# Kernel tuning notes

Hardware: AMD Instinct MI355X
Metric: run time of the kernel (lower is better)

## Reference

```python
import jax, jax.numpy as jnp
import numpy as np

# Mamba2 config (matches mamba_ssm.Mamba2 defaults used by the wrapper)
D_MODEL = 1024
D_STATE = 128
D_CONV = 4
EXPAND = 2
HEADDIM = 64
CHUNK = 256
D_INNER = EXPAND * D_MODEL            # 2048
NHEADS = D_INNER // HEADDIM           # 32
CONV_DIM = D_INNER + 2 * D_STATE      # 2304 (x, B, C share the causal conv)
D_IN_PROJ = 2 * D_INNER + 2 * D_STATE + NHEADS  # z, xBC, dt
EPS = 1e-5


def rmsnorm(x, w, eps=EPS):
    return x * jax.lax.rsqrt(jnp.mean(x * x, axis=-1, keepdims=True) + eps) * w


def setup_inputs() -> dict:
    key = jax.random.key(0)
    ks = jax.random.split(key, 8)
    B, L = 2, 2048
    def w(k, shape, sc=0.02):
        return jax.random.normal(k, shape, jnp.float32) * sc
    return {
        "x": jax.random.normal(ks[0], (B, L, D_MODEL), jnp.float32),
        "norm_w": jnp.ones((D_MODEL,), jnp.float32),
        "in_proj_w": w(ks[1], (D_IN_PROJ, D_MODEL)),
        "conv_w": w(ks[2], (CONV_DIM, 1, D_CONV), 0.2),   # depthwise kernel
        "conv_b": jnp.zeros((CONV_DIM,), jnp.float32),
        "dt_bias": w(ks[3], (NHEADS,), 1.0),
        "A_log": jnp.log(1.0 + 15.0 * jax.random.uniform(ks[4], (NHEADS,), jnp.float32)),
        "D": jnp.ones((NHEADS,), jnp.float32),
        "gnorm_w": jnp.ones((D_INNER,), jnp.float32),
        "out_proj_w": w(ks[5], (D_MODEL, D_INNER)),
    }


def _ssd(xd, a, Bm, Cm):
    """Chunked SSD scan (ssd_minimal_discrete).
    xd: (b,l,h,p) = x*dt ; a: (b,l,h) = dt*A ; Bm,Cm: (b,l,n) (ngroups=1)."""
    b, l, h, p = xd.shape
    n = Bm.shape[-1]
    nc = l // CHUNK
    xd = xd.reshape(b, nc, CHUNK, h, p)
    a = a.reshape(b, nc, CHUNK, h).transpose(0, 3, 1, 2)   # (b,h,nc,c)
    Bm = Bm.reshape(b, nc, CHUNK, n)
    Cm = Cm.reshape(b, nc, CHUNK, n)
    a_cs = jnp.cumsum(a, axis=-1)                           # (b,h,nc,c)
    # 1) intra-chunk: causal decay matrix L[t,s] = exp(sum_{s<i<=t} a_i)
    diff = a_cs[..., :, None] - a_cs[..., None, :]          # (b,h,nc,c,c)
    mask = jnp.tril(jnp.ones((CHUNK, CHUNK), bool))
    Lm = jnp.exp(jnp.where(mask, diff, 0.0)) * mask
    Y_diag = jnp.einsum("bcln,bcsn,bhcls,bcshp->bclhp", Cm, Bm, Lm, xd)
    # 2) per-chunk end states
    decay_states = jnp.exp(a_cs[..., -1:] - a_cs)           # (b,h,nc,c)
    states = jnp.einsum("bcln,bhcl,bclhp->bchpn", Bm, decay_states, xd)
    # 3) inter-chunk recurrence (vectorized segsum over the 8+1 chunk totals)
    tot = jnp.pad(a_cs[..., -1], ((0, 0), (0, 0), (1, 0)))  # (b,h,nc+1)
    tot_cs = jnp.cumsum(tot, axis=-1)
    dchunk = tot_cs[..., :, None] - tot_cs[..., None, :]    # (b,h,nc+1,nc+1)
    cmask = jnp.tril(jnp.ones((nc + 1, nc + 1), bool))
    dchunk = jnp.exp(jnp.where(cmask, dchunk, 0.0)) * cmask
    states = jnp.concatenate([jnp.zeros_like(states[:, :1]), states], axis=1)
    new_states = jnp.einsum("bhzc,bchpn->bzhpn", dchunk, states)
    init_states = new_states[:, :-1]                        # state entering each chunk
    # 4) state -> output contribution
    Y_off = jnp.einsum("bcln,bchpn,bhcl->bclhp", Cm, init_states, jnp.exp(a_cs))
    return (Y_diag + Y_off).reshape(b, l, h, p)


def reference(x, norm_w, in_proj_w, conv_w, conv_b, dt_bias, A_log, D, gnorm_w, out_proj_w):
    res = x
    u = rmsnorm(x, norm_w)
    zxbcdt = u @ in_proj_w.T                                # (b,l,d_in_proj)
    z, xBC, dt = jnp.split(zxbcdt, [D_INNER, D_INNER + CONV_DIM], axis=-1)
    # causal depthwise conv1d over (x,B,C), then SiLU
    xBC_t = jnp.pad(xBC.transpose(0, 2, 1), ((0, 0), (0, 0), (D_CONV - 1, 0)))
    conv = jax.lax.conv_general_dilated(
        xBC_t, conv_w, (1,), "VALID",
        dimension_numbers=("NCH", "OIH", "NCH"), feature_group_count=CONV_DIM)
    xBC = jax.nn.silu(conv.transpose(0, 2, 1) + conv_b)
    xs, Bm, Cm = jnp.split(xBC, [D_INNER, D_INNER + D_STATE], axis=-1)
    dt = jax.nn.softplus(dt + dt_bias)                      # (b,l,h)
    A = -jnp.exp(A_log)                                     # (h,)
    xh = xs.reshape(xs.shape[0], xs.shape[1], NHEADS, HEADDIM)
    y = _ssd(xh * dt[..., None], dt * A, Bm, Cm)
    y = y + D[None, None, :, None] * xh                     # skip term
    y = y.reshape(xs.shape)
    y = rmsnorm(y * jax.nn.silu(z), gnorm_w)                # gated RMSNorm
    return res + y @ out_proj_w.T
```

## Files before the change

kernel.cpp:

```cpp
#include <hip/hip_runtime.h>
#include <hip/hip_bf16.h>

typedef __hip_bfloat16 bf16_t;
typedef __attribute__((ext_vector_type(8))) short bfrag8;
typedef __attribute__((ext_vector_type(4))) float floatx4;

#define DM     1024
#define DI     2048
#define NHD    32
#define HD     64
#define DSTATE 128
#define CONVD  2304
#define NPROJ  4384
#define NPAD   4480
#define MR     4096
#define LL     2048
#define EPSF   1e-5f
#define PSTR   40
#define LOG2E  1.44269504088896f

__device__ __forceinline__ void gl_lds16(const void* g, void* l) {
  __builtin_amdgcn_global_load_lds((const __attribute__((address_space(1))) void*)g,
                                   (__attribute__((address_space(3))) void*)l, 16, 0, 0);
}
__device__ __forceinline__ unsigned pack_bf16_rn(float a, float b) {
  unsigned ua = (__float_as_uint(a) + 0x8000u) >> 16;
  unsigned ub = (__float_as_uint(b) + 0x8000u) >> 16;
  return ua | (ub << 16);
}
__device__ __forceinline__ unsigned short bf16u(float a) {
  return (unsigned short)((__float_as_uint(a) + 0x8000u) >> 16);
}
__device__ __forceinline__ float blo(unsigned u){ return __uint_as_float(u << 16); }
__device__ __forceinline__ float bhi(unsigned u){ return __uint_as_float(u & 0xffff0000u); }
__device__ __forceinline__ void unp8(uint4 u, float* v) {
  v[0]=blo(u.x); v[1]=bhi(u.x); v[2]=blo(u.y); v[3]=bhi(u.y);
  v[4]=blo(u.z); v[5]=bhi(u.z); v[6]=blo(u.w); v[7]=bhi(u.w);
}

__global__ void rms1_kernel(const float* __restrict__ x, const float* __restrict__ w,
                            bf16_t* __restrict__ ub) {
  int row = blockIdx.x, t = threadIdx.x;
  float4 v = ((const float4*)(x + (long)row * DM))[t];
  float ss = v.x*v.x + v.y*v.y + v.z*v.z + v.w*v.w;
#pragma unroll
  for (int off = 32; off > 0; off >>= 1) ss += __shfl_down(ss, off, 64);
  __shared__ float red[4];
  if ((t & 63) == 0) red[t >> 6] = ss;
  __syncthreads();
  float tot = red[0] + red[1] + red[2] + red[3];
  float rs = rsqrtf(tot * (1.f / DM) + EPSF);
  float4 wv = ((const float4*)w)[t];
  bf16_t* o = ub + (long)row * DM + t * 4;
  o[0] = __float2bfloat16(v.x * rs * wv.x);
  o[1] = __float2bfloat16(v.y * rs * wv.y);
  o[2] = __float2bfloat16(v.z * rs * wv.z);
  o[3] = __float2bfloat16(v.w * rs * wv.w);
}

#define W1CNT (NPAD * DM / 4)
#define W2CNT (DM * DI / 4)
__global__ void cvtw_kernel(const float* __restrict__ w1, const float* __restrict__ w2,
                            const float* __restrict__ gw,
                            bf16_t* __restrict__ o1, bf16_t* __restrict__ o2) {
  int i4 = blockIdx.x * 256 + threadIdx.x;
  if (i4 < W1CNT) {
    int idx = i4 * 4;
    int row = idx >> 10;
    float4 v = make_float4(0.f, 0.f, 0.f, 0.f);
    if (row < NPROJ) v = *(const float4*)(w1 + idx);
    bf16_t* d = o1 + idx;
    d[0] = __float2bfloat16(v.x); d[1] = __float2bfloat16(v.y);
    d[2] = __float2bfloat16(v.z); d[3] = __float2bfloat16(v.w);
  } else {
    int idx = (i4 - W1CNT) * 4;
    int k = idx & (DI - 1);
    float4 v = *(const float4*)(w2 + idx);
    float4 g = *(const float4*)(gw + k);
    bf16_t* d = o2 + idx;
    d[0] = __float2bfloat16(v.x * g.x); d[1] = __float2bfloat16(v.y * g.y);
    d[2] = __float2bfloat16(v.z * g.z); d[3] = __float2bfloat16(v.w * g.w);
  }
}

template<int TN, bool DO_RES, bool OUT_BF16>
__global__ __launch_bounds__(256) void gemm64_kernel(const bf16_t* __restrict__ A,
    const bf16_t* __restrict__ Bw, const float* __restrict__ resid,
    const float* __restrict__ rs_row, void* __restrict__ Cout, int N, int K) {
  __shared__ bf16_t As[128 * 64];
  __shared__ bf16_t Bs[TN * 64];
  const int tid = threadIdx.x;
  const int lane = tid & 63;
  const int wv = tid >> 6;
  const int l15 = lane & 15;
  const int l4 = lane >> 4;
  constexpr int MF = (TN == 128) ? 4 : 2;
  const int wm = (TN == 128) ? ((wv >> 1) << 6) : (wv << 5);
  const int wn = (TN == 128) ? ((wv & 1) << 6) : 0;
  const int tm = blockIdx.x << 7;
  const int tn = blockIdx.y * TN;

  floatx4 acc[MF][4];
#pragma unroll
  for (int i = 0; i < MF; i++)
#pragma unroll
    for (int j = 0; j < 4; j++) acc[i][j] = (floatx4){0.f, 0.f, 0.f, 0.f};

  const int r = tid >> 3;
  const int c8 = tid & 7;
  const int scol = ((c8 ^ (r & 7)) << 3);
  const bf16_t* Ag = A + (long)(tm + r) * K + scol;
  const bf16_t* Bg = Bw + (long)(tn + r) * K + scol;
  const int swz = l15 & 7;

  for (int k0 = 0; k0 < K; k0 += 64) {
#pragma unroll
    for (int q = 0; q < 4; q++)
      gl_lds16(Ag + (long)(q * 32) * K + k0, &As[q * 2048 + tid * 8]);
#pragma unroll
    for (int q = 0; q < TN / 32; q++)
      gl_lds16(Bg + (long)(q * 32) * K + k0, &Bs[q * 2048 + tid * 8]);
    __syncthreads();
#pragma unroll
    for (int kk = 0; kk < 2; kk++) {
      bfrag8 af[MF], bfr[4];
      const int ch = ((kk << 2) | l4) ^ swz;
#pragma unroll
      for (int j = 0; j < 4; j++)
        bfr[j] = *(const bfrag8*)&Bs[(wn + j * 16 + l15) * 64 + ch * 8];
#pragma unroll
      for (int i = 0; i < MF; i++)
        af[i] = *(const bfrag8*)&As[(wm + i * 16 + l15) * 64 + ch * 8];
#pragma unroll
      for (int i = 0; i < MF; i++)
#pragma unroll
        for (int j = 0; j < 4; j++)
          acc[i][j] = __builtin_amdgcn_mfma_f32_16x16x32_bf16(af[i], bfr[j], acc[i][j], 0, 0, 0);
    }
    __syncthreads();
  }
#pragma unroll
  for (int i = 0; i < MF; i++)
#pragma unroll
    for (int j = 0; j < 4; j++)
#pragma unroll
      for (int r2 = 0; r2 < 4; r2++) {
        int row = tm + wm + i * 16 + l4 * 4 + r2;
        int col = tn + wn + j * 16 + l15;
        float v = acc[i][j][r2];
        if (OUT_BF16) {
          ((bf16_t*)Cout)[(long)row * N + col] = __float2bfloat16(v);
        } else {
          if (DO_RES) v = v * rs_row[row] + resid[(long)row * N + col];
          ((float*)Cout)[(long)row * N + col] = v;
        }
      }
}

__global__ __launch_bounds__(256) void gemm_s_kernel(const bf16_t* __restrict__ Cmh,
                const bf16_t* __restrict__ Bmh, float* __restrict__ SL) {
  __shared__ bf16_t As[128 * 32];
  __shared__ bf16_t Bs[128 * 32];
  const int tid = threadIdx.x;
  const int lane = tid & 63;
  const int wv = tid >> 6;
  const int wm = (wv >> 1) << 6;
  const int wn = (wv & 1) << 6;
  const int bc = blockIdx.z;
  const int tm = blockIdx.x << 7;
  const int tn = blockIdx.y << 7;
  const int l15 = lane & 15;
  const int l4 = lane >> 4;
  floatx4 acc[4][4];
#pragma unroll
  for (int i = 0; i < 4; i++)
#pragma unroll
    for (int j = 0; j < 4; j++) acc[i][j] = (floatx4){0.f, 0.f, 0.f, 0.f};
  const int arow = tid >> 2;
  const int acol = (tid & 3) << 3;
  const bf16_t* Ag = Cmh + (long)bc * 256 * DSTATE + (long)(tm + arow) * DSTATE + acol;
  const bf16_t* Bg = Bmh + (long)bc * 256 * DSTATE + (long)(tn + arow) * DSTATE + acol;
  const long k64 = (long)64 * DSTATE;
  for (int k0 = 0; k0 < DSTATE; k0 += 32) {
    gl_lds16(Ag + k0, &As[tid * 8]);
    gl_lds16(Ag + k64 + k0, &As[2048 + tid * 8]);
    gl_lds16(Bg + k0, &Bs[tid * 8]);
    gl_lds16(Bg + k64 + k0, &Bs[2048 + tid * 8]);
    __syncthreads();
    bfrag8 af[4], bfr[4];
#pragma unroll
    for (int i = 0; i < 4; i++)
      af[i] = *(const bfrag8*)&As[(wm + i * 16 + l15) * 32 + l4 * 8];
#pragma unroll
    for (int j = 0; j < 4; j++)
      bfr[j] = *(const bfrag8*)&Bs[(wn + j * 16 + l15) * 32 + l4 * 8];
#pragma unroll
    for (int i = 0; i < 4; i++)
#pragma unroll
      for (int j = 0; j < 4; j++)
        acc[i][j] = __builtin_amdgcn_mfma_f32_16x16x32_bf16(af[i], bfr[j], acc[i][j], 0, 0, 0);
    __syncthreads();
  }
  float* Cb = SL + (long)bc * 65536;
#pragma unroll
  for (int i = 0; i < 4; i++)
#pragma unroll
    for (int j = 0; j < 4; j++)
#pragma unroll
      for (int r = 0; r < 4; r++)
        Cb[(long)(tm + wm + i * 16 + l4 * 4 + r) * 256 + tn + wn + j * 16 + l15] = acc[i][j][r];
}

__global__ __launch_bounds__(256) void conv4_kernel(const bf16_t* __restrict__ zxh,
    const float* __restrict__ cw, const float* __restrict__ cb,
    bf16_t* __restrict__ xhb, bf16_t* __restrict__ Bmh, bf16_t* __restrict__ Cmh) {
  int g = blockIdx.x * 256 + threadIdx.x;
  int cg = g % 288;
  int blt = g / 288;
  int c0 = cg * 8;
  long bl0 = (long)blt * 4;
  int l0 = (int)(bl0 & (LL - 1));
  const bf16_t* base = zxh + bl0 * NPAD + DI + c0;
  float rv[7][8];
#pragma unroll
  for (int j = 0; j < 7; j++) {
    int dj = j - 3;
    if (l0 + dj >= 0) {
      uint4 u = *(const uint4*)(base + (long)dj * NPAD);
      unp8(u, rv[j]);
    } else {
#pragma unroll
      for (int q = 0; q < 8; q++) rv[j][q] = 0.f;
    }
  }
  float4 wq[8];
#pragma unroll
  for (int q = 0; q < 8; q++) wq[q] = ((const float4*)cw)[c0 + q];
  float bias[8];
  *(float4*)&bias[0] = *(const float4*)(cb + c0);
  *(float4*)&bias[4] = *(const float4*)(cb + c0 + 4);
#pragma unroll
  for (int i = 0; i < 4; i++) {
    unsigned o[4];
#pragma unroll
    for (int q2 = 0; q2 < 4; q2++) {
      float rr[2];
#pragma unroll
      for (int e = 0; e < 2; e++) {
        int q = q2 * 2 + e;
        float a = bias[q] + wq[q].x * rv[i][q] + wq[q].y * rv[i + 1][q]
                + wq[q].z * rv[i + 2][q] + wq[q].w * rv[i + 3][q];
        rr[e] = a / (1.f + __expf(-a));
      }
      o[q2] = pack_bf16_rn(rr[0], rr[1]);
    }
    uint4 ov = make_uint4(o[0], o[1], o[2], o[3]);
    long bl = bl0 + i;
    if (c0 < DI)               *(uint4*)(xhb + bl * DI + c0) = ov;
    else if (c0 < DI + DSTATE) *(uint4*)(Bmh + bl * DSTATE + (c0 - DI)) = ov;
    else                       *(uint4*)(Cmh + bl * DSTATE + (c0 - DI - DSTATE)) = ov;
  }
}

__global__ __launch_bounds__(256) void xdt_kernel(const bf16_t* __restrict__ xhb,
    const bf16_t* __restrict__ Bmh, const bf16_t* __restrict__ zxh,
    const float* __restrict__ A_log, const float* __restrict__ dtb,
    float* __restrict__ acs, float* __restrict__ ctot,
    bf16_t* __restrict__ xdT, bf16_t* __restrict__ xdTe, bf16_t* __restrict__ BmT) {
  __shared__ unsigned short Tb[9216];
  __shared__ float acsL[256];
  __shared__ float dtsL[256];
  __shared__ float wsum[4];
  int blk = blockIdx.x;
  int t = threadIdx.x;
  if (blk < 512) {
    int h = blk & 31, bc = blk >> 5;
    {
      int lane = t & 63, w = t >> 6;
      float Ah = -__expf(A_log[h]) * LOG2E;
      int gl = bc * 256 + t;
      float vv = __bfloat162float(zxh[(long)gl * NPAD + (NPROJ - 32) + h]) + dtb[h];
      float sp = fmaxf(vv, 0.f) + log1pf(__expf(-fabsf(vv)));
      float a = sp * Ah;
#pragma unroll
      for (int off = 1; off < 64; off <<= 1) {
        float v = __shfl_up(a, off, 64);
        if (lane >= off) a += v;
      }
      if (lane == 63) wsum[w] = a;
      __syncthreads();
      float base = 0.f;
      for (int i = 0; i < 4; i++) base += (i < w) ? wsum[i] : 0.f;
      a += base;
      acsL[t] = a;
      dtsL[t] = sp;
      acs[blk * 256 + t] = a;
      if (t == 255) ctot[blk] = a;
      __syncthreads();
    }
    float atot = acsL[255];
    unsigned short* T1 = Tb;
    unsigned short* T2 = Tb + 4608;
    int l_loc = t >> 2, pg = t & 3;
    for (int lt = 0; lt < 4; lt++) {
      int ll = lt * 64 + l_loc;
      int gl = bc * 256 + ll;
      float w1 = dtsL[ll];
      float w2 = w1 * exp2f(atot - acsL[ll]);
      const uint4* src = (const uint4*)(xhb + (long)gl * DI + h * HD + pg * 16);
      uint4 u0 = src[0], u1 = src[1];
      float v[16];
      unp8(u0, v); unp8(u1, v + 8);
      __syncthreads();
#pragma unroll
      for (int q = 0; q < 16; q++) {
        T1[(pg * 16 + q) * 72 + l_loc] = bf16u(v[q] * w1);
        T2[(pg * 16 + q) * 72 + l_loc] = bf16u(v[q] * w2);
      }
      __syncthreads();
      long orow = ((long)blk * 64 + l_loc) * 256 + lt * 64 + pg * 16;
      *(uint4*)(xdT + orow)      = *(uint4*)&T1[l_loc * 72 + pg * 16];
      *(uint4*)(xdT + orow + 8)  = *(uint4*)&T1[l_loc * 72 + pg * 16 + 8];
      *(uint4*)(xdTe + orow)     = *(uint4*)&T2[l_loc * 72 + pg * 16];
      *(uint4*)(xdTe + orow + 8) = *(uint4*)&T2[l_loc * 72 + pg * 16 + 8];
    }
  } else {
    unsigned short* T = Tb;
    int bc = blk - 512;
    int l_loc = t >> 2, ng = t & 3;
    for (int lt = 0; lt < 4; lt++) {
      int gl = bc * 256 + lt * 64 + l_loc;
      const uint4* src = (const uint4*)(Bmh + (long)gl * DSTATE + ng * 32);
      uint4 u[4];
#pragma unroll
      for (int q = 0; q < 4; q++) u[q] = src[q];
      __syncthreads();
      const unsigned short* us = (const unsigned short*)u;
#pragma unroll
      for (int e = 0; e < 32; e++)
        T[(ng * 32 + e) * 72 + l_loc] = us[e];
      __syncthreads();
      int n = t >> 1, lg2 = t & 1;
      long orow = ((long)bc * 128 + n) * 256 + lt * 64 + lg2 * 32;
#pragma unroll
      for (int q = 0; q < 4; q++)
        *(uint4*)(BmT + orow + q * 8) = *(uint4*)&T[n * 72 + lg2 * 32 + q * 8];
    }
  }
}

__global__ __launch_bounds__(256) void states3_kernel(const bf16_t* __restrict__ xdTe,
    const bf16_t* __restrict__ BmT, bf16_t* __restrict__ states) {
  int blk = blockIdx.x;
  int bc = blk >> 5;
  int t = threadIdx.x, lane = t & 63, wv = t >> 6;
  int l15 = lane & 15, l4 = lane >> 4;
  floatx4 acc[2][4];
#pragma unroll
  for (int i = 0; i < 2; i++)
#pragma unroll
    for (int j = 0; j < 4; j++) acc[i][j] = (floatx4){0.f, 0.f, 0.f, 0.f};
  const bf16_t* arow = BmT + (long)bc * 128 * 256;
  const bf16_t* brow = xdTe + (long)blk * 64 * 256;
#pragma unroll
  for (int kt = 0; kt < 8; kt++) {
    bfrag8 af[2], bfr[4];
#pragma unroll
    for (int i = 0; i < 2; i++)
      af[i] = *(const bfrag8*)(arow + (long)(wv * 32 + i * 16 + l15) * 256 + kt * 32 + l4 * 8);
#pragma unroll
    for (int j = 0; j < 4; j++)
      bfr[j] = *(const bfrag8*)(brow + (long)(j * 16 + l15) * 256 + kt * 32 + l4 * 8);
#pragma unroll
    for (int i = 0; i < 2; i++)
#pragma unroll
      for (int j = 0; j < 4; j++)
        acc[i][j] = __builtin_amdgcn_mfma_f32_16x16x32_bf16(af[i], bfr[j], acc[i][j], 0, 0, 0);
  }
#pragma unroll
  for (int i = 0; i < 2; i++)
#pragma unroll
    for (int j = 0; j < 4; j++) {
      int n_base = wv * 32 + i * 16 + l4 * 4;
      int p = j * 16 + l15;
      unsigned lo = pack_bf16_rn(acc[i][j][0], acc[i][j][1]);
      unsigned hi = pack_bf16_rn(acc[i][j][2], acc[i][j][3]);
      *(uint2*)(states + (long)blk * 8192 + p * 128 + n_base) = make_uint2(lo, hi);
    }
}

__global__ void scan_kernel(const bf16_t* __restrict__ states, const float* __restrict__ ctot,
                            bf16_t* __restrict__ initsb) {
  int id = blockIdx.x * 256 + threadIdx.x;
  int pn = id & 8191;
  int bh = id >> 13;
  int b = bh >> 5, h = bh & 31;
  float S = 0.f;
#pragma unroll
  for (int c = 0; c < 8; c++) {
    int blk = (b * 8 + c) * 32 + h;
    initsb[(long)blk * 8192 + pn] = __float2bfloat16(S);
    S = exp2f(ctot[blk]) * S + __bfloat162float(states[(long)blk * 8192 + pn]);
  }
}

__global__ __launch_bounds__(256) void yk3_kernel(const float* __restrict__ SL,
     const bf16_t* __restrict__ Cmh, const bf16_t* __restrict__ xhb,
     const bf16_t* __restrict__ zxh, const float* __restrict__ acs,
     const bf16_t* __restrict__ initsb, const bf16_t* __restrict__ xdT,
     const float* __restrict__ Dp, bf16_t* __restrict__ yg, float* __restrict__ ssqp) {
  int bi = blockIdx.x;
  int mh = bi & 1, h = (bi >> 1) & 31, bc = bi >> 6;
  int ablk = bc * 32 + h;
  int t = threadIdx.x;
  int lane = t & 63, wv = t >> 6;
  int l15 = lane & 15, l4 = lane >> 4;
  __shared__ float acsS[256];
  __shared__ bf16_t Ps[128 * PSTR];
  __shared__ __align__(16) char bbuf[49152];
  bf16_t* xds = (bf16_t*)bbuf;
  bf16_t* ins = (bf16_t*)(bbuf + 32768);
  float* Yt = (float*)bbuf;

  {
    const bf16_t* xrow_g = xdT + (long)ablk * 64 * 256;
#pragma unroll
    for (int it = 0; it < 8; it++) {
      int sl = it * 256 + t;
      int p = sl >> 5, s = sl & 31;
      int c = (s & 24) | ((s & 7) ^ (p & 7));
      gl_lds16(xrow_g + p * 256 + c * 8, &xds[sl * 8]);
    }
    const bf16_t* irow_g = initsb + (long)ablk * 8192;
#pragma unroll
    for (int it = 0; it < 4; it++) {
      int sl = it * 256 + t;
      int p = sl >> 4, s = sl & 15;
      int c = (s & 8) | ((s & 7) ^ (p & 7));
      gl_lds16(irow_g + p * 128 + c * 8, &ins[sl * 8]);
    }
  }
  acsS[t] = acs[ablk * 256 + t];
  __syncthreads();

  const int l_loc = t >> 1, half = t & 1;
  const int l = mh * 128 + l_loc;
  const float al = acsS[l];
  const float eAl = exp2f(al);
  const int rowbase = bc * 256;
  const float* SLb = SL + (long)bc * 65536 + (long)l * 256;

  floatx4 acc[2][4];
#pragma unroll
  for (int i = 0; i < 2; i++)
#pragma unroll
    for (int j = 0; j < 4; j++) acc[i][j] = (floatx4){0.f, 0.f, 0.f, 0.f};

  const int nkd = (mh + 1) * 4;
  float4 slv[4];
#pragma unroll
  for (int q = 0; q < 4; q++) slv[q] = ((const float4*)(SLb + half * 16))[q];

  for (int kt = 0; kt < nkd + 4; kt++) {
    unsigned pk[8];
    if (kt < nkd) {
      int s0 = kt * 32 + half * 16;
#pragma unroll
      for (int q = 0; q < 4; q++) {
        float4 v = slv[q];
        int sb = s0 + q * 4;
        float p0 = (sb + 0 <= l) ? v.x * exp2f(al - acsS[sb + 0]) : 0.f;
        float p1 = (sb + 1 <= l) ? v.y * exp2f(al - acsS[sb + 1]) : 0.f;
        float p2 = (sb + 2 <= l) ? v.z * exp2f(al - acsS[sb + 2]) : 0.f;
        float p3 = (sb + 3 <= l) ? v.w * exp2f(al - acsS[sb + 3]) : 0.f;
        pk[q * 2 + 0] = pack_bf16_rn(p0, p1);
        pk[q * 2 + 1] = pack_bf16_rn(p2, p3);
      }
    } else {
      int n0 = (kt - nkd) * 32;
      const uint4* Cg = (const uint4*)(Cmh + (long)(rowbase + l) * DSTATE + n0 + half * 16);
      uint4 u0 = Cg[0], u1 = Cg[1];
      float cv[16];
      unp8(u0, cv); unp8(u1, cv + 8);
#pragma unroll
      for (int q = 0; q < 8; q++)
        pk[q] = pack_bf16_rn(cv[q * 2] * eAl, cv[q * 2 + 1] * eAl);
    }
    {
      uint4* pw = (uint4*)&Ps[l_loc * PSTR + half * 16];
      pw[0] = make_uint4(pk[0], pk[1], pk[2], pk[3]);
      pw[1] = make_uint4(pk[4], pk[5], pk[6], pk[7]);
    }
    if (kt + 1 < nkd) {
#pragma unroll
      for (int q = 0; q < 4; q++)
        slv[q] = ((const float4*)(SLb + (kt + 1) * 32 + half * 16))[q];
    }
    __syncthreads();
    bfrag8 bfr[4];
    if (kt < nkd) {
      int ch = kt * 4 + l4;
#pragma unroll
      for (int j = 0; j < 4; j++) {
        int p = j * 16 + l15;
        int sw = (ch & 24) | ((ch & 7) ^ (p & 7));
        bfr[j] = *(const bfrag8*)&xds[(p * 32 + sw) * 8];
      }
    } else {
      int ch = (kt - nkd) * 4 + l4;
#pragma unroll
      for (int j = 0; j < 4; j++) {
        int p = j * 16 + l15;
        int sw = (ch & 8) | ((ch & 7) ^ (p & 7));
        bfr[j] = *(const bfrag8*)&ins[(p * 16 + sw) * 8];
      }
    }
#pragma unroll
    for (int i = 0; i < 2; i++) {
      bfrag8 af = *(const bfrag8*)&Ps[(wv * 32 + i * 16 + l15) * PSTR + l4 * 8];
#pragma unroll
      for (int j = 0; j < 4; j++)
        acc[i][j] = __builtin_amdgcn_mfma_f32_16x16x32_bf16(af, bfr[j], acc[i][j], 0, 0, 0);
    }
    __syncthreads();
  }
#pragma unroll
  for (int i = 0; i < 2; i++)
#pragma unroll
    for (int j = 0; j < 4; j++)
#pragma unroll
      for (int r = 0; r < 4; r++)
        Yt[(wv * 32 + i * 16 + l4 * 4 + r) * 66 + j * 16 + l15] = acc[i][j][r];
  __syncthreads();
  {
    int row_l = t >> 1;
    int ch = (t & 1) * 32;
    long rowg = rowbase + mh * 128 + row_l;
    float Dh = Dp[h];
    float ss = 0.f;
#pragma unroll
    for (int it = 0; it < 4; it++) {
      int c = ch + it * 8;
      float4 y0 = *(const float4*)&Yt[row_l * 66 + c];
      float4 y1 = *(const float4*)&Yt[row_l * 66 + c + 4];
      uint4 ux = *(const uint4*)(xhb + rowg * DI + h * HD + c);
      uint4 uz = *(const uint4*)(zxh + rowg * NPAD + h * HD + c);
      float xv[8], zv[8];
      unp8(ux, xv); unp8(uz, zv);
      float yv[8] = {y0.x, y0.y, y0.z, y0.w, y1.x, y1.y, y1.z, y1.w};
      unsigned o[4];
#pragma unroll
      for (int q = 0; q < 4; q++) {
        float v0 = (yv[q * 2 + 0] + Dh * xv[q * 2 + 0]) *
                   (zv[q * 2 + 0] / (1.f + __expf(-zv[q * 2 + 0])));
        float v1 = (yv[q * 2 + 1] + Dh * xv[q * 2 + 1]) *
                   (zv[q * 2 + 1] / (1.f + __expf(-zv[q * 2 + 1])));
        ss += v0 * v0 + v1 * v1;
        o[q] = pack_bf16_rn(v0, v1);
      }
      *(uint4*)(yg + rowg * DI + h * HD + c) = make_uint4(o[0], o[1], o[2], o[3]);
    }
    ss += __shfl_xor(ss, 1, 64);
    if ((t & 1) == 0) ssqp[rowg * 32 + h] = ss;
  }
}

__global__ void rsred_kernel(const float* __restrict__ ssqp, float* __restrict__ rs) {
  int row = blockIdx.x * 256 + threadIdx.x;
  const float4* p = (const float4*)(ssqp + row * 32);
  float s = 0.f;
#pragma unroll
  for (int q = 0; q < 8; q++) {
    float4 v = p[q];
    s += v.x + v.y + v.z + v.w;
  }
  rs[row] = rsqrtf(s * (1.f / DI) + EPSF);
}

extern "C" void kernel_launch(void* const* d_in, const int* in_sizes, int n_in,
                              void* d_out, int out_size, void* d_ws, size_t ws_size,
                              hipStream_t stream) {
  const float* x    = (const float*)d_in[0];
  const float* nw   = (const float*)d_in[1];
  const float* w1   = (const float*)d_in[2];
  const float* cw   = (const float*)d_in[3];
  const float* cb   = (const float*)d_in[4];
  const float* dtb  = (const float*)d_in[5];
  const float* alog = (const float*)d_in[6];
  const float* Dp   = (const float*)d_in[7];
  const float* gw   = (const float*)d_in[8];
  const float* w2   = (const float*)d_in[9];
  float* out = (float*)d_out;

  char* ws = (char*)d_ws;
  size_t off = 0;
  auto alloc = [&](size_t bytes) -> void* {
    void* p = ws + off;
    off += (bytes + 255) & ~(size_t)255;
    return p;
  };
  bf16_t* ub     = (bf16_t*)alloc((size_t)MR * DM * 2);
  bf16_t* w1b    = (bf16_t*)alloc((size_t)NPAD * DM * 2);
  bf16_t* w2b    = (bf16_t*)alloc((size_t)DM * DI * 2);
  bf16_t* zxh    = (bf16_t*)alloc((size_t)MR * NPAD * 2);
  bf16_t* xhb    = (bf16_t*)alloc((size_t)MR * DI * 2);
  bf16_t* Bmh    = (bf16_t*)alloc((size_t)MR * DSTATE * 2);
  bf16_t* Cmh    = (bf16_t*)alloc((size_t)MR * DSTATE * 2);
  float* SL      = (float*)alloc((size_t)16 * 256 * 256 * 4);
  float* acs     = (float*)alloc((size_t)512 * 256 * 4);
  float* ctot    = (float*)alloc((size_t)512 * 4);
  bf16_t* states = (bf16_t*)alloc((size_t)512 * 8192 * 2);
  bf16_t* initsb = (bf16_t*)alloc((size_t)512 * 8192 * 2);
  bf16_t* xdT    = (bf16_t*)alloc((size_t)512 * 64 * 256 * 2);
  bf16_t* xdTe   = (bf16_t*)alloc((size_t)512 * 64 * 256 * 2);
  bf16_t* BmT    = (bf16_t*)alloc((size_t)16 * 128 * 256 * 2);
  bf16_t* yg     = (bf16_t*)alloc((size_t)MR * DI * 2);
  float* ssqp    = (float*)alloc((size_t)MR * NHD * 4);
  float* rs      = (float*)alloc((size_t)MR * 4);
  if (off > ws_size) return;

  rms1_kernel<<<MR, 256, 0, stream>>>(x, nw, ub);
  cvtw_kernel<<<(W1CNT + W2CNT) / 256, 256, 0, stream>>>(w1, w2, gw, w1b, w2b);
  gemm64_kernel<128, false, true><<<dim3(MR / 128, NPAD / 128), 256, 0, stream>>>(
      ub, w1b, nullptr, nullptr, zxh, NPAD, DM);
  conv4_kernel<<<(1024 * 288) / 256, 256, 0, stream>>>(zxh, cw, cb, xhb, Bmh, Cmh);
  xdt_kernel<<<528, 256, 0, stream>>>(xhb, Bmh, zxh, alog, dtb, acs, ctot, xdT, xdTe, BmT);
  gemm_s_kernel<<<dim3(2, 2, 16), 256, 0, stream>>>(Cmh, Bmh, SL);
  states3_kernel<<<512, 256, 0, stream>>>(xdTe, BmT, states);
  scan_kernel<<<(2 * 32 * 8192) / 256, 256, 0, stream>>>(states, ctot, initsb);
  yk3_kernel<<<1024, 256, 0, stream>>>(SL, Cmh, xhb, zxh, acs, initsb, xdT, Dp, yg, ssqp);
  rsred_kernel<<<MR / 256, 256, 0, stream>>>(ssqp, rs);
  gemm64_kernel<64, true, false><<<dim3(MR / 128, DM / 64), 256, 0, stream>>>(
      yg, w2b, x, rs, out, DM, DI);
}
```

Measured before the change: 282.7 us.

## Merge yk kernel halves into one 512-thread block with register-built A fragments

The Y-output kernel now uses one 512-thread block per (chunk, head), with both 128-row halves in the same block. The shared xd and initial-state tiles are therefore loaded into LDS once instead of twice. A fragments (decay-weighted scores and scaled C) are built directly in registers in MFMA layout rather than staged through an LDS buffer, which removes the per-iteration barriers. The epilogue writes Y through LDS in two passes. Costs are higher register pressure per thread, two extra barriers in the epilogue, and a changed block-to-chunk ordering.

```diff
diff --git a/kernel.cpp b/kernel.cpp
--- a/kernel.cpp
+++ b/kernel.cpp
@@ -16,7 +16,6 @@
 #define MR     4096
 #define LL     2048
 #define EPSF   1e-5f
-#define PSTR   40
 #define LOG2E  1.44269504088896f
 
 __device__ __forceinline__ void gl_lds16(const void* g, void* l) {
@@ -37,6 +36,7 @@
   v[0]=blo(u.x); v[1]=bhi(u.x); v[2]=blo(u.y); v[3]=bhi(u.y);
   v[4]=blo(u.z); v[5]=bhi(u.z); v[6]=blo(u.w); v[7]=bhi(u.w);
 }
+typedef union { unsigned u[4]; bfrag8 f; } fragu;
 
 __global__ void rms1_kernel(const float* __restrict__ x, const float* __restrict__ w,
                             bf16_t* __restrict__ ub) {
@@ -404,19 +404,22 @@
   }
 }
 
-__global__ __launch_bounds__(256) void yk3_kernel(const float* __restrict__ SL,
+__global__ __launch_bounds__(512, 4) void yk4_kernel(const float* __restrict__ SL,
      const bf16_t* __restrict__ Cmh, const bf16_t* __restrict__ xhb,
      const bf16_t* __restrict__ zxh, const float* __restrict__ acs,
      const bf16_t* __restrict__ initsb, const bf16_t* __restrict__ xdT,
      const float* __restrict__ Dp, bf16_t* __restrict__ yg, float* __restrict__ ssqp) {
   int bi = blockIdx.x;
-  int mh = bi & 1, h = (bi >> 1) & 31, bc = bi >> 6;
+  int bc = (bi & 7) * 2 + ((bi >> 3) & 1);
+  int h = bi >> 4;
   int ablk = bc * 32 + h;
   int t = threadIdx.x;
-  int lane = t & 63, wv = t >> 6;
+  int wv = t >> 6;
+  int mh = wv >> 2, wsub = wv & 3;
+  int lane = t & 63;
   int l15 = lane & 15, l4 = lane >> 4;
+
   __shared__ float acsS[256];
-  __shared__ bf16_t Ps[128 * PSTR];
   __shared__ __align__(16) char bbuf[49152];
   bf16_t* xds = (bf16_t*)bbuf;
   bf16_t* ins = (bf16_t*)(bbuf + 32768);
@@ -425,30 +428,31 @@
   {
     const bf16_t* xrow_g = xdT + (long)ablk * 64 * 256;
 #pragma unroll
-    for (int it = 0; it < 8; it++) {
-      int sl = it * 256 + t;
+    for (int it = 0; it < 4; it++) {
+      int sl = it * 512 + t;
       int p = sl >> 5, s = sl & 31;
       int c = (s & 24) | ((s & 7) ^ (p & 7));
       gl_lds16(xrow_g + p * 256 + c * 8, &xds[sl * 8]);
     }
     const bf16_t* irow_g = initsb + (long)ablk * 8192;
 #pragma unroll
-    for (int it = 0; it < 4; it++) {
-      int sl = it * 256 + t;
+    for (int it = 0; it < 2; it++) {
+      int sl = it * 512 + t;
       int p = sl >> 4, s = sl & 15;
       int c = (s & 8) | ((s & 7) ^ (p & 7));
       gl_lds16(irow_g + p * 128 + c * 8, &ins[sl * 8]);
     }
   }
-  acsS[t] = acs[ablk * 256 + t];
+  if (t < 256) acsS[t] = acs[ablk * 256 + t];
   __syncthreads();
 
-  const int l_loc = t >> 1, half = t & 1;
-  const int l = mh * 128 + l_loc;
-  const float al = acsS[l];
-  const float eAl = exp2f(al);
   const int rowbase = bc * 256;
-  const float* SLb = SL + (long)bc * 65536 + (long)l * 256;
+  const int l0 = mh * 128 + wsub * 32 + l15;
+  const int l1 = l0 + 16;
+  const float al0 = acsS[l0], al1 = acsS[l1];
+  const float eA0 = exp2f(al0), eA1 = exp2f(al1);
+  const float* SL0 = SL + (long)bc * 65536 + (long)l0 * 256;
+  const float* SL1 = SL + (long)bc * 65536 + (long)l1 * 256;
 
   floatx4 acc[2][4];
 #pragma unroll
@@ -457,111 +461,118 @@
     for (int j = 0; j < 4; j++) acc[i][j] = (floatx4){0.f, 0.f, 0.f, 0.f};
 
   const int nkd = (mh + 1) * 4;
-  float4 slv[4];
-#pragma unroll
-  for (int q = 0; q < 4; q++) slv[q] = ((const float4*)(SLb + half * 16))[q];
-
-  for (int kt = 0; kt < nkd + 4; kt++) {
-    unsigned pk[8];
-    if (kt < nkd) {
-      int s0 = kt * 32 + half * 16;
-#pragma unroll
-      for (int q = 0; q < 4; q++) {
-        float4 v = slv[q];
-        int sb = s0 + q * 4;
-        float p0 = (sb + 0 <= l) ? v.x * exp2f(al - acsS[sb + 0]) : 0.f;
-        float p1 = (sb + 1 <= l) ? v.y * exp2f(al - acsS[sb + 1]) : 0.f;
-        float p2 = (sb + 2 <= l) ? v.z * exp2f(al - acsS[sb + 2]) : 0.f;
-        float p3 = (sb + 3 <= l) ? v.w * exp2f(al - acsS[sb + 3]) : 0.f;
-        pk[q * 2 + 0] = pack_bf16_rn(p0, p1);
-        pk[q * 2 + 1] = pack_bf16_rn(p2, p3);
+  for (int kt = 0; kt < nkd; kt++) {
+    int sbase = kt * 32 + l4 * 8;
+    float as[8];
+    *(float4*)&as[0] = *(const float4*)&acsS[sbase];
+    *(float4*)&as[4] = *(const float4*)&acsS[sbase + 4];
+    float sv0[8], sv1[8];
+    *(float4*)&sv0[0] = *(const float4*)(SL0 + sbase);
+    *(float4*)&sv0[4] = *(const float4*)(SL0 + sbase + 4);
+    *(float4*)&sv1[0] = *(const float4*)(SL1 + sbase);
+    *(float4*)&sv1[4] = *(const float4*)(SL1 + sbase + 4);
+    fragu af0, af1;
+#pragma unroll
+    for (int q2 = 0; q2 < 4; q2++) {
+      float p00, p01, p10, p11;
+      {
+        int s = sbase + q2 * 2;
+        float d0 = al0 - as[q2 * 2], d1 = al0 - as[q2 * 2 + 1];
+        p00 = (s <= l0) ? sv0[q2 * 2] * exp2f(fminf(d0, 0.f)) : 0.f;
+        p01 = (s + 1 <= l0) ? sv0[q2 * 2 + 1] * exp2f(fminf(d1, 0.f)) : 0.f;
+        float e0 = al1 - as[q2 * 2], e1 = al1 - as[q2 * 2 + 1];
+        p10 = (s <= l1) ? sv1[q2 * 2] * exp2f(fminf(e0, 0.f)) : 0.f;
+        p11 = (s + 1 <= l1) ? sv1[q2 * 2 + 1] * exp2f(fminf(e1, 0.f)) : 0.f;
       }
-    } else {
-      int n0 = (kt - nkd) * 32;
-      const uint4* Cg = (const uint4*)(Cmh + (long)(rowbase + l) * DSTATE + n0 + half * 16);
-      uint4 u0 = Cg[0], u1 = Cg[1];
-      float cv[16];
-      unp8(u0, cv); unp8(u1, cv + 8);
-#pragma unroll
-      for (int q = 0; q < 8; q++)
-        pk[q] = pack_bf16_rn(cv[q * 2] * eAl, cv[q * 2 + 1] * eAl);
-    }
+      af0.u[q2] = pack_bf16_rn(p00, p01);
+      af1.u[q2] = pack_bf16_rn(p10, p11);
+    }
+    bfrag8 bfr[4];
+    int ch = kt * 4 + l4;
+#pragma unroll
+    for (int j = 0; j < 4; j++) {
+      int p = j * 16 + l15;
+      int sw = (ch & 24) | ((ch & 7) ^ (p & 7));
+      bfr[j] = *(const bfrag8*)&xds[(p * 32 + sw) * 8];
+    }
+#pragma unroll
+    for (int j = 0; j < 4; j++) {
+      acc[0][j] = __builtin_amdgcn_mfma_f32_16x16x32_bf16(af0.f, bfr[j], acc[0][j], 0, 0, 0);
+      acc[1][j] = __builtin_amdgcn_mfma_f32_16x16x32_bf16(af1.f, bfr[j], acc[1][j], 0, 0, 0);
+    }
+  }
+#pragma unroll
+  for (int kt = 0; kt < 4; kt++) {
+    int n0 = kt * 32 + l4 * 8;
+    uint4 c0 = *(const uint4*)(Cmh + (long)(rowbase + l0) * DSTATE + n0);
+    uint4 c1 = *(const uint4*)(Cmh + (long)(rowbase + l1) * DSTATE + n0);
+    float cv0[8], cv1[8];
+    unp8(c0, cv0); unp8(c1, cv1);
+    fragu af0, af1;
+#pragma unroll
+    for (int q2 = 0; q2 < 4; q2++) {
+      af0.u[q2] = pack_bf16_rn(cv0[q2 * 2] * eA0, cv0[q2 * 2 + 1] * eA0);
+      af1.u[q2] = pack_bf16_rn(cv1[q2 * 2] * eA1, cv1[q2 * 2 + 1] * eA1);
+    }
+    bfrag8 bfr[4];
+    int ch = kt * 4 + l4;
+#pragma unroll
+    for (int j = 0; j < 4; j++) {
+      int p = j * 16 + l15;
+      int sw = (ch & 8) | ((ch & 7) ^ (p & 7));
+      bfr[j] = *(const bfrag8*)&ins[(p * 16 + sw) * 8];
+    }
+#pragma unroll
+    for (int j = 0; j < 4; j++) {
+      acc[0][j] = __builtin_amdgcn_mfma_f32_16x16x32_bf16(af0.f, bfr[j], acc[0][j], 0, 0, 0);
+      acc[1][j] = __builtin_amdgcn_mfma_f32_16x16x32_bf16(af1.f, bfr[j], acc[1][j], 0, 0, 0);
+    }
+  }
+  float Dh = Dp[h];
+#pragma unroll
+  for (int pass = 0; pass < 2; pass++) {
+    __syncthreads();
+    if (mh == pass) {
+#pragma unroll
+      for (int i = 0; i < 2; i++)
+#pragma unroll
+        for (int j = 0; j < 4; j++)
+#pragma unroll
+          for (int r = 0; r < 4; r++)
+            Yt[(wsub * 32 + i * 16 + l4 * 4 + r) * 66 + j * 16 + l15] = acc[i][j][r];
+    }
+    __syncthreads();
     {
-      uint4* pw = (uint4*)&Ps[l_loc * PSTR + half * 16];
-      pw[0] = make_uint4(pk[0], pk[1], pk[2], pk[3]);
-      pw[1] = make_uint4(pk[4], pk[5], pk[6], pk[7]);
-    }
-    if (kt + 1 < nkd) {
-#pragma unroll
-      for (int q = 0; q < 4; q++)
-        slv[q] = ((const float4*)(SLb + (kt + 1) * 32 + half * 16))[q];
-    }
-    __syncthreads();
-    bfrag8 bfr[4];
-    if (kt < nkd) {
-      int ch = kt * 4 + l4;
-#pragma unroll
-      for (int j = 0; j < 4; j++) {
-        int p = j * 16 + l15;
-        int sw = (ch & 24) | ((ch & 7) ^ (p & 7));
-        bfr[j] = *(const bfrag8*)&xds[(p * 32 + sw) * 8];
+      int row_l = t >> 2;
+      int chc = (t & 3) * 16;
+      long rowg = rowbase + pass * 128 + row_l;
+      float ss = 0.f;
+#pragma unroll
+      for (int it = 0; it < 2; it++) {
+        int c = chc + it * 8;
+        float4 y0 = *(const float4*)&Yt[row_l * 66 + c];
+        float4 y1 = *(const float4*)&Yt[row_l * 66 + c + 4];
+        uint4 ux = *(const uint4*)(xhb + rowg * DI + h * HD + c);
+        uint4 uz = *(const uint4*)(zxh + rowg * NPAD + h * HD + c);
+        float xv[8], zv[8];
+        unp8(ux, xv); unp8(uz, zv);
+        float yv[8] = {y0.x, y0.y, y0.z, y0.w, y1.x, y1.y, y1.z, y1.w};
+        unsigned o[4];
+#pragma unroll
+        for (int q = 0; q < 4; q++) {
+          float v0 = (yv[q * 2 + 0] + Dh * xv[q * 2 + 0]) *
+                     (zv[q * 2 + 0] / (1.f + __expf(-zv[q * 2 + 0])));
+          float v1 = (yv[q * 2 + 1] + Dh * xv[q * 2 + 1]) *
+                     (zv[q * 2 + 1] / (1.f + __expf(-zv[q * 2 + 1])));
+          ss += v0 * v0 + v1 * v1;
+          o[q] = pack_bf16_rn(v0, v1);
+        }
+        *(uint4*)(yg + rowg * DI + h * HD + c) = make_uint4(o[0], o[1], o[2], o[3]);
       }
-    } else {
-      int ch = (kt - nkd) * 4 + l4;
-#pragma unroll
-      for (int j = 0; j < 4; j++) {
-        int p = j * 16 + l15;
-        int sw = (ch & 8) | ((ch & 7) ^ (p & 7));
-        bfr[j] = *(const bfrag8*)&ins[(p * 16 + sw) * 8];
-      }
-    }
-#pragma unroll
-    for (int i = 0; i < 2; i++) {
-      bfrag8 af = *(const bfrag8*)&Ps[(wv * 32 + i * 16 + l15) * PSTR + l4 * 8];
-#pragma unroll
-      for (int j = 0; j < 4; j++)
-        acc[i][j] = __builtin_amdgcn_mfma_f32_16x16x32_bf16(af, bfr[j], acc[i][j], 0, 0, 0);
-    }
-    __syncthreads();
-  }
-#pragma unroll
-  for (int i = 0; i < 2; i++)
-#pragma unroll
-    for (int j = 0; j < 4; j++)
-#pragma unroll
-      for (int r = 0; r < 4; r++)
-        Yt[(wv * 32 + i * 16 + l4 * 4 + r) * 66 + j * 16 + l15] = acc[i][j][r];
-  __syncthreads();
-  {
-    int row_l = t >> 1;
-    int ch = (t & 1) * 32;
-    long rowg = rowbase + mh * 128 + row_l;
-    float Dh = Dp[h];
-    float ss = 0.f;
-#pragma unroll
-    for (int it = 0; it < 4; it++) {
-      int c = ch + it * 8;
-      float4 y0 = *(const float4*)&Yt[row_l * 66 + c];
-      float4 y1 = *(const float4*)&Yt[row_l * 66 + c + 4];
-      uint4 ux = *(const uint4*)(xhb + rowg * DI + h * HD + c);
-      uint4 uz = *(const uint4*)(zxh + rowg * NPAD + h * HD + c);
-      float xv[8], zv[8];
-      unp8(ux, xv); unp8(uz, zv);
-      float yv[8] = {y0.x, y0.y, y0.z, y0.w, y1.x, y1.y, y1.z, y1.w};
-      unsigned o[4];
-#pragma unroll
-      for (int q = 0; q < 4; q++) {
-        float v0 = (yv[q * 2 + 0] + Dh * xv[q * 2 + 0]) *
-                   (zv[q * 2 + 0] / (1.f + __expf(-zv[q * 2 + 0])));
-        float v1 = (yv[q * 2 + 1] + Dh * xv[q * 2 + 1]) *
-                   (zv[q * 2 + 1] / (1.f + __expf(-zv[q * 2 + 1])));
-        ss += v0 * v0 + v1 * v1;
-        o[q] = pack_bf16_rn(v0, v1);
-      }
-      *(uint4*)(yg + rowg * DI + h * HD + c) = make_uint4(o[0], o[1], o[2], o[3]);
-    }
-    ss += __shfl_xor(ss, 1, 64);
-    if ((t & 1) == 0) ssqp[rowg * 32 + h] = ss;
+      ss += __shfl_xor(ss, 1, 64);
+      ss += __shfl_xor(ss, 2, 64);
+      if ((t & 3) == 0) ssqp[rowg * 32 + h] = ss;
+    }
   }
 }
 
@@ -628,7 +639,7 @@
   gemm_s_kernel<<<dim3(2, 2, 16), 256, 0, stream>>>(Cmh, Bmh, SL);
   states3_kernel<<<512, 256, 0, stream>>>(xdTe, BmT, states);
   scan_kernel<<<(2 * 32 * 8192) / 256, 256, 0, stream>>>(states, ctot, initsb);
-  yk3_kernel<<<1024, 256, 0, stream>>>(SL, Cmh, xhb, zxh, acs, initsb, xdT, Dp, yg, ssqp);
+  yk4_kernel<<<512, 512, 0, stream>>>(SL, Cmh, xhb, zxh, acs, initsb, xdT, Dp, yg, ssqp);
   rsred_kernel<<<MR / 256, 256, 0, stream>>>(ssqp, rs);
   gemm64_kernel<64, true, false><<<dim3(MR / 128, DM / 64), 256, 0, stream>>>(
       yg, w2b, x, rs, out, DM, DI);
```

After: 265.8 us. 6.0% less time.
